# Kernel tuning notes

Measured on AMD Instinct MI355X. Metric: run time of the kernel, lower is better.

## Reference

```python
import jax, jax.numpy as jnp
import numpy as np

EPS = 1e-5

def layer_norm(x, gamma, beta):
    mu = jnp.mean(x, axis=-1, keepdims=True)
    var = jnp.var(x, axis=-1, keepdims=True)
    return (x - mu) * jax.lax.rsqrt(var + EPS) * gamma + beta

def setup_inputs() -> dict:
    key = jax.random.key(0)
    ks = jax.random.split(key, 9)
    B, S, H = 4, 4096, 1024
    x = jax.random.normal(ks[0], (B, S, H), dtype=jnp.float32)
    w1 = jax.random.normal(ks[1], (H, 4 * H), dtype=jnp.float32) * (1.0 / np.sqrt(H))
    b1 = jnp.zeros((4 * H,), dtype=jnp.float32)
    w2 = jax.random.normal(ks[2], (4 * H, H), dtype=jnp.float32) * (1.0 / np.sqrt(4 * H))
    b2 = jnp.zeros((H,), dtype=jnp.float32)
    g1 = jnp.ones((H,), dtype=jnp.float32)
    be1 = jnp.zeros((H,), dtype=jnp.float32)
    g2 = jnp.ones((H,), dtype=jnp.float32)
    be2 = jnp.zeros((H,), dtype=jnp.float32)
    return {"x": x, "w1": w1, "b1": b1, "w2": w2, "b2": b2,
            "g1": g1, "be1": be1, "g2": g2, "be2": be2}

def reference(x, w1, b1, w2, b2, g1, be1, g2, be2):
    # FNet mixing: FFT over hidden dim, then seq dim, take real part
    x_ft = jnp.fft.fft(jnp.fft.fft(x.astype(jnp.float32), axis=-1), axis=-2).real
    h = layer_norm(x + x_ft, g1, be1)
    # FFN with exact GELU (torch nn.GELU default); dropout is identity in eval
    ffn = jax.nn.gelu(h @ w1 + b1, approximate=False) @ w2 + b2
    return layer_norm(h + ffn, g2, be2)
```

## Files before the change

### kernel.cpp

```cpp
#include <hip/hip_runtime.h>
#include <math.h>
#include <stdint.h>

#define DI __device__ __forceinline__
typedef unsigned short u16;
typedef unsigned int   u32;
typedef unsigned long long u64;

typedef __attribute__((ext_vector_type(4))) float f32x4;
typedef __attribute__((ext_vector_type(8))) short bf16x8;

DI float bf2f(u16 v){ return __uint_as_float(((u32)v) << 16); }
DI u16 f2bf(float f){ u32 u = __float_as_uint(f); return (u16)((u + 0x7FFFu + ((u >> 16) & 1u)) >> 16); }
DI u32 pack2(float re, float im){ return (u32)f2bf(re) | ((u32)f2bf(im) << 16); }

DI float gelu_fast(float v){
  float t = v * v;
  float z = v * fmaf(0.0356774081f, t, 0.7978845608f);
  z = fminf(z, 15.0f);
  float e = __expf(2.0f * z);
  return v * e * __frcp_rn(1.0f + e);
}

__global__ __launch_bounds__(256) void transpose_u32(const u32* __restrict__ in, u32* __restrict__ out, int R, int C){
  __shared__ u32 tile[64][65];
  int t = threadIdx.x;
  int c = t & 63, r0 = t >> 6;
  size_t bofs = (size_t)blockIdx.z * (size_t)R * (size_t)C;
  const u32* ib = in  + bofs + (size_t)(blockIdx.y * 64) * C + blockIdx.x * 64;
  u32*       ob = out + bofs + (size_t)(blockIdx.x * 64) * R + blockIdx.y * 64;
  #pragma unroll
  for (int i = 0; i < 16; i++){ int r = r0 + i * 4; tile[r][c] = ib[(size_t)r * C + c]; }
  __syncthreads();
  #pragma unroll
  for (int i = 0; i < 16; i++){ int r = r0 + i * 4; ob[(size_t)r * R + c] = tile[c][r]; }
}

__global__ __launch_bounds__(256) void transpose_f32_bf16(const float* __restrict__ in, u16* __restrict__ out, int R, int C){
  __shared__ u16 tile[64][65];
  int t = threadIdx.x;
  int c = t & 63, r0 = t >> 6;
  const float* ib = in  + (size_t)(blockIdx.y * 64) * C + blockIdx.x * 64;
  u16*         ob = out + (size_t)(blockIdx.x * 64) * R + blockIdx.y * 64;
  #pragma unroll
  for (int i = 0; i < 16; i++){ int r = r0 + i * 4; tile[r][c] = f2bf(ib[(size_t)r * C + c]); }
  __syncthreads();
  #pragma unroll
  for (int i = 0; i < 16; i++){ int r = r0 + i * 4; ob[(size_t)r * R + c] = tile[c][r]; }
}

template<int LOGN>
DI float2* fft_r4(float2* s, float2* d, int t){
  const int Q = 1 << (LOGN - 2);
  #pragma unroll
  for (int st = 0; st < (LOGN >> 1); ++st){
    const int m = 1 << (2 * st);
    const float ang = -6.28318530717958647692f * (float)m / (float)(1 << LOGN);
    #pragma unroll
    for (int j0 = 0; j0 < Q; j0 += 256){
      int j = j0 + t;
      int p = j >> (2 * st);
      int q = j & (m - 1);
      int o = q + (p << (2 * st + 2));
      float2 a0 = s[j], a1 = s[j + Q], a2 = s[j + 2 * Q], a3 = s[j + 3 * Q];
      float s0r = a0.x + a2.x, s0i = a0.y + a2.y, d0r = a0.x - a2.x, d0i = a0.y - a2.y;
      float s1r = a1.x + a3.x, s1i = a1.y + a3.y, d1r = a1.x - a3.x, d1i = a1.y - a3.y;
      float sn, cs; __sincosf(ang * (float)p, &sn, &cs);
      float t2r = cs * cs - sn * sn, t2i = 2.f * cs * sn;
      float t3r = t2r * cs - t2i * sn, t3i = t2r * sn + t2i * cs;
      float e1r = d0r + d1i, e1i = d0i - d1r;
      float e2r = s0r - s1r, e2i = s0i - s1i;
      float e3r = d0r - d1i, e3i = d0i + d1r;
      d[o]         = make_float2(s0r + s1r, s0i + s1i);
      d[o + m]     = make_float2(cs * e1r - sn * e1i,  cs * e1i + sn * e1r);
      d[o + 2 * m] = make_float2(t2r * e2r - t2i * e2i, t2r * e2i + t2i * e2r);
      d[o + 3 * m] = make_float2(t3r * e3r - t3i * e3i, t3r * e3i + t3i * e3r);
    }
    __syncthreads();
    float2* tp = s; s = d; d = tp;
  }
  return s;
}

__global__ __launch_bounds__(256) void fft_seq(const float* __restrict__ xT, u32* __restrict__ ZT2,
                                               float* __restrict__ Zny){
  __shared__ float2 A[4096], Bb[4096];
  int t = threadIdx.x, g = blockIdx.x;
  const float* r0 = xT + (size_t)(2 * g) * 4096;
  #pragma unroll
  for (int i = 0; i < 4; i++){
    int idx = i * 1024 + t * 4;
    float4 va = *(const float4*)(r0 + idx);
    float4 vb = *(const float4*)(r0 + 4096 + idx);
    A[idx + 0] = make_float2(va.x, vb.x);
    A[idx + 1] = make_float2(va.y, vb.y);
    A[idx + 2] = make_float2(va.z, vb.z);
    A[idx + 3] = make_float2(va.w, vb.w);
  }
  __syncthreads();
  float2* R = fft_r4<12>(A, Bb, t);
  size_t ob0 = (size_t)(2 * g) * 2048;
  #pragma unroll
  for (int i = 0; i < 2; i++){
    int k0 = i * 1024 + t * 4;
    u32 wa[4], wb[4];
    #pragma unroll
    for (int kk = 0; kk < 4; kk++){
      int k = k0 + kk, m = (4096 - k) & 4095;
      float2 zk = R[k], zm = R[m];
      wa[kk] = pack2(0.5f * (zk.x + zm.x), 0.5f * (zk.y - zm.y));
      wb[kk] = pack2(0.5f * (zk.y + zm.y), 0.5f * (zm.x - zk.x));
    }
    *(uint4*)(ZT2 + ob0 + k0)        = make_uint4(wa[0], wa[1], wa[2], wa[3]);
    *(uint4*)(ZT2 + ob0 + 2048 + k0) = make_uint4(wb[0], wb[1], wb[2], wb[3]);
  }
  if (t == 0){ float2 z = R[2048]; Zny[2 * g] = z.x; Zny[2 * g + 1] = z.y; }
}

DI void block_stats4(float a1, float a2, float b1, float b2, int t,
                     float& mA, float& iA, float& mB, float& iB){
  __shared__ float sh[4][4];
  #pragma unroll
  for (int o = 32; o > 0; o >>= 1){
    a1 += __shfl_down(a1, o); a2 += __shfl_down(a2, o);
    b1 += __shfl_down(b1, o); b2 += __shfl_down(b2, o);
  }
  if ((t & 63) == 0){ int w = t >> 6; sh[w][0] = a1; sh[w][1] = a2; sh[w][2] = b1; sh[w][3] = b2; }
  __syncthreads();
  float SA = sh[0][0] + sh[1][0] + sh[2][0] + sh[3][0];
  float QA = sh[0][1] + sh[1][1] + sh[2][1] + sh[3][1];
  float SB = sh[0][2] + sh[1][2] + sh[2][2] + sh[3][2];
  float QB = sh[0][3] + sh[1][3] + sh[2][3] + sh[3][3];
  mA = SA * (1.f / 1024.f); iA = rsqrtf(QA * (1.f / 1024.f) - mA * mA + 1e-5f);
  mB = SB * (1.f / 1024.f); iB = rsqrtf(QB * (1.f / 1024.f) - mB * mB + 1e-5f);
}

__global__ __launch_bounds__(256) void fft_hid_ln(const u32* __restrict__ Z2, const float* __restrict__ Zny,
    const float* __restrict__ x, const float* __restrict__ g1, const float* __restrict__ be1,
    u16* __restrict__ h){
  __shared__ float2 A[1024], Bb[1024];
  int t = threadIdx.x, id = blockIdx.x;
  int b = id / 2049, k = id - b * 2049;
  int idx = t * 4;
  if (k == 2048){
    float4 v = *(const float4*)(Zny + b * 1024 + idx);
    A[idx + 0] = make_float2(v.x, 0.f); A[idx + 1] = make_float2(v.y, 0.f);
    A[idx + 2] = make_float2(v.z, 0.f); A[idx + 3] = make_float2(v.w, 0.f);
  } else {
    uint4 zv = *(const uint4*)(Z2 + ((size_t)b * 2048 + k) * 1024 + idx);
    A[idx + 0] = make_float2(bf2f((u16)(zv.x & 0xffffu)), bf2f((u16)(zv.x >> 16)));
    A[idx + 1] = make_float2(bf2f((u16)(zv.y & 0xffffu)), bf2f((u16)(zv.y >> 16)));
    A[idx + 2] = make_float2(bf2f((u16)(zv.z & 0xffffu)), bf2f((u16)(zv.z >> 16)));
    A[idx + 3] = make_float2(bf2f((u16)(zv.w & 0xffffu)), bf2f((u16)(zv.w >> 16)));
  }
  __syncthreads();
  float2* R = fft_r4<10>(A, Bb, t);
  int rowA = b * 4096 + k;
  bool two = (k >= 1) && (k <= 2047);
  int rowB = b * 4096 + (4096 - k);
  float4 xa = *(const float4*)(x + (size_t)rowA * 1024 + idx);
  float vA0 = R[idx + 0].x + xa.x, vA1 = R[idx + 1].x + xa.y;
  float vA2 = R[idx + 2].x + xa.z, vA3 = R[idx + 3].x + xa.w;
  float vB0 = 0.f, vB1 = 0.f, vB2 = 0.f, vB3 = 0.f;
  if (two){
    float4 xb = *(const float4*)(x + (size_t)rowB * 1024 + idx);
    vB0 = R[(1024 - (idx + 0)) & 1023].x + xb.x;
    vB1 = R[(1024 - (idx + 1)) & 1023].x + xb.y;
    vB2 = R[(1024 - (idx + 2)) & 1023].x + xb.z;
    vB3 = R[(1024 - (idx + 3)) & 1023].x + xb.w;
  }
  float mA, iA, mB, iB;
  block_stats4(vA0 + vA1 + vA2 + vA3, vA0 * vA0 + vA1 * vA1 + vA2 * vA2 + vA3 * vA3,
               vB0 + vB1 + vB2 + vB3, vB0 * vB0 + vB1 * vB1 + vB2 * vB2 + vB3 * vB3,
               t, mA, iA, mB, iB);
  float4 gv = *(const float4*)(g1 + idx);
  float4 bv = *(const float4*)(be1 + idx);
  ushort4 oA;
  oA.x = f2bf((vA0 - mA) * iA * gv.x + bv.x);
  oA.y = f2bf((vA1 - mA) * iA * gv.y + bv.y);
  oA.z = f2bf((vA2 - mA) * iA * gv.z + bv.z);
  oA.w = f2bf((vA3 - mA) * iA * gv.w + bv.w);
  *(ushort4*)(h + (size_t)rowA * 1024 + idx) = oA;
  if (two){
    ushort4 oB;
    oB.x = f2bf((vB0 - mB) * iB * gv.x + bv.x);
    oB.y = f2bf((vB1 - mB) * iB * gv.y + bv.y);
    oB.z = f2bf((vB2 - mB) * iB * gv.z + bv.z);
    oB.w = f2bf((vB3 - mB) * iB * gv.w + bv.w);
    *(ushort4*)(h + (size_t)rowB * 1024 + idx) = oB;
  }
}

__global__ __launch_bounds__(256) void ln_rows(const u16* __restrict__ yv, const float* __restrict__ g,
    const float* __restrict__ be, float* __restrict__ o){
  int t = threadIdx.x;
  size_t base = (size_t)blockIdx.x * 1024;
  int idx = t * 4;
  ushort4 v4 = *(const ushort4*)(yv + base + idx);
  float v0 = bf2f(v4.x), v1 = bf2f(v4.y), v2 = bf2f(v4.z), v3 = bf2f(v4.w);
  float mA, iA, mB, iB;
  block_stats4(v0 + v1 + v2 + v3, v0 * v0 + v1 * v1 + v2 * v2 + v3 * v3, 0.f, 0.f, t, mA, iA, mB, iB);
  float4 gv = *(const float4*)(g + idx);
  float4 bv = *(const float4*)(be + idx);
  float4 ov;
  ov.x = (v0 - mA) * iA * gv.x + bv.x;
  ov.y = (v1 - mA) * iA * gv.y + bv.y;
  ov.z = (v2 - mA) * iA * gv.z + bv.z;
  ov.w = (v3 - mA) * iA * gv.w + bv.w;
  *(float4*)(o + base + idx) = ov;
}

typedef const __attribute__((address_space(1))) void* as1cp;
typedef __attribute__((address_space(3))) void* as3p;
DI void async_copy16(const void* g, void* l){
  __builtin_amdgcn_global_load_lds((as1cp)(u64)g, (as3p)(u32)(u64)l, 16, 0, 0);
}
DI void bar(){
  asm volatile("" ::: "memory");
  __builtin_amdgcn_s_barrier();
  asm volatile("" ::: "memory");
}

template<int DOGELU>
__global__ __launch_bounds__(512, 2) void gemm256(const u16* __restrict__ A, const u16* __restrict__ Bm,
    const float* __restrict__ bias, const u16* __restrict__ resid, u16* __restrict__ C,
    int M, int N, int K, int npg_shift)
{
  __shared__ u16 sA[2][2][8192];
  __shared__ u16 sB[2][2][8192];
  int t = threadIdx.x, wv = t >> 6, ln = t & 63;

  int bid = blockIdx.x;
  int c8 = bid & 7, j = bid >> 3;
  int ng = c8 & 3, mh = c8 >> 2;
  int npg = 1 << npg_shift;
  int mph = (M >> 8) >> 1;
  int n0 = (((ng << npg_shift) + (j & (npg - 1))) << 8);
  int m0 = ((mh * mph + (j >> npg_shift)) << 8);

  int wm = wv >> 2, wn = wv & 3;
  int lt = ln & 15;
  int cs = (((ln >> 4) ^ ((ln >> 1) & 3)) << 3);
  int arow = (wm * 128 + lt) * 32 + cs;
  int brow = (wn * 64 + lt) * 32 + cs;

  int srow = wv * 32 + (ln >> 2);
  int gch  = ((ln & 3) ^ ((srow >> 1) & 3)) << 3;
  const u16* gA0 = A  + (size_t)(m0 + srow) * K + gch;
  const u16* gA1 = gA0 + (size_t)16 * K;
  const u16* gB0 = Bm + (size_t)(n0 + srow) * K + gch;
  const u16* gB1 = gB0 + (size_t)16 * K;
  int ldof = wv * 1024 + ln * 8;

  #define STAGE(g0, g1, kc, unit) do{ \
    async_copy16((g0) + (kc), (unit) + ldof); \
    async_copy16((g1) + (kc), (unit) + 512 + ldof); }while(0)

  f32x4 acc[8][4];
  #pragma unroll
  for (int mf = 0; mf < 8; mf++)
    #pragma unroll
    for (int nf = 0; nf < 4; nf++) acc[mf][nf] = (f32x4){0.f, 0.f, 0.f, 0.f};

  int NT = K >> 6;

  STAGE(gA0, gA1, 0,  &sA[0][0][0]);
  STAGE(gB0, gB1, 0,  &sB[0][0][0]);
  STAGE(gA0, gA1, 32, &sA[0][1][0]);
  STAGE(gB0, gB1, 32, &sB[0][1][0]);
  STAGE(gA0, gA1, 64, &sA[1][0][0]);
  STAGE(gB0, gB1, 64, &sB[1][0][0]);
  STAGE(gA0, gA1, 96, &sA[1][1][0]);
  asm volatile("s_waitcnt vmcnt(6)" ::: "memory");
  bar();

  for (int kt = 0; kt < NT; ++kt){
    int buf = kt & 1;
    u16* a0s = &sA[buf][0][0];
    u16* a1s = &sA[buf][1][0];
    u16* b0s = &sB[buf][0][0];
    u16* b1s = &sB[buf][1][0];
    u16* bn1 = &sB[buf ^ 1][1][0];
    bool st1 = (kt + 1) < NT;
    bool st2 = (kt + 2) < NT;
    int kb1 = (kt + 1) << 6, kb2 = (kt + 2) << 6;
    bf16x8 af[8], b0r, b1r, b2r, b3r;

    #pragma unroll
    for (int mf = 0; mf < 8; mf++) af[mf] = *(const bf16x8*)(a0s + arow + mf * 512);
    b0r = *(const bf16x8*)(b0s + brow);
    b1r = *(const bf16x8*)(b0s + brow + 512);
    if (st1) STAGE(gB0, gB1, kb1 + 32, bn1);
    bar();
    __builtin_amdgcn_s_setprio(1);
    #pragma unroll
    for (int mf = 0; mf < 8; mf++){
      acc[mf][0] = __builtin_amdgcn_mfma_f32_16x16x32_bf16(af[mf], b0r, acc[mf][0], 0, 0, 0);
      acc[mf][1] = __builtin_amdgcn_mfma_f32_16x16x32_bf16(af[mf], b1r, acc[mf][1], 0, 0, 0);
    }
    __builtin_amdgcn_s_setprio(0);
    bar();

    b2r = *(const bf16x8*)(b0s + brow + 1024);
    b3r = *(const bf16x8*)(b0s + brow + 1536);
    if (st2) STAGE(gA0, gA1, kb2, a0s);
    bar();
    __builtin_amdgcn_s_setprio(1);
    #pragma unroll
    for (int mf = 0; mf < 8; mf++){
      acc[mf][2] = __builtin_amdgcn_mfma_f32_16x16x32_bf16(af[mf], b2r, acc[mf][2], 0, 0, 0);
      acc[mf][3] = __builtin_amdgcn_mfma_f32_16x16x32_bf16(af[mf], b3r, acc[mf][3], 0, 0, 0);
    }
    __builtin_amdgcn_s_setprio(0);
    bar();

    #pragma unroll
    for (int mf = 0; mf < 8; mf++) af[mf] = *(const bf16x8*)(a1s + arow + mf * 512);
    b0r = *(const bf16x8*)(b1s + brow);
    b1r = *(const bf16x8*)(b1s + brow + 512);
    if (st2) STAGE(gB0, gB1, kb2, b0s);
    bar();
    __builtin_amdgcn_s_setprio(1);
    #pragma unroll
    for (int mf = 0; mf < 8; mf++){
      acc[mf][0] = __builtin_amdgcn_mfma_f32_16x16x32_bf16(af[mf], b0r, acc[mf][0], 0, 0, 0);
      acc[mf][1] = __builtin_amdgcn_mfma_f32_16x16x32_bf16(af[mf], b1r, acc[mf][1], 0, 0, 0);
    }
    __builtin_amdgcn_s_setprio(0);
    bar();

    b2r = *(const bf16x8*)(b1s + brow + 1024);
    b3r = *(const bf16x8*)(b1s + brow + 1536);
    if (st2) STAGE(gA0, gA1, kb2 + 32, a1s);
    bar();
    __builtin_amdgcn_s_setprio(1);
    #pragma unroll
    for (int mf = 0; mf < 8; mf++){
      acc[mf][2] = __builtin_amdgcn_mfma_f32_16x16x32_bf16(af[mf], b2r, acc[mf][2], 0, 0, 0);
      acc[mf][3] = __builtin_amdgcn_mfma_f32_16x16x32_bf16(af[mf], b3r, acc[mf][3], 0, 0, 0);
    }
    __builtin_amdgcn_s_setprio(0);
    if (st2) asm volatile("s_waitcnt vmcnt(6)" ::: "memory");
    else     asm volatile("s_waitcnt vmcnt(0)" ::: "memory");
    bar();
  }
  #undef STAGE

  int colq = lt, rq = ln >> 4;
  #pragma unroll
  for (int mf = 0; mf < 8; mf++){
    int mr = m0 + wm * 128 + mf * 16 + rq * 4;
    #pragma unroll
    for (int nf = 0; nf < 4; nf++){
      int col = n0 + wn * 64 + nf * 16 + colq;
      float bv = bias[col];
      #pragma unroll
      for (int i = 0; i < 4; i++){
        float v = acc[mf][nf][i] + bv;
        if (DOGELU){
          v = gelu_fast(v);
        } else {
          v += bf2f(resid[(size_t)(mr + i) * N + col]);
        }
        C[(size_t)(mr + i) * N + col] = f2bf(v);
      }
    }
  }
}

extern "C" void kernel_launch(void* const* d_in, const int* in_sizes, int n_in,
                              void* d_out, int out_size, void* d_ws, size_t ws_size,
                              hipStream_t stream){
  const float* x   = (const float*)d_in[0];
  const float* w1  = (const float*)d_in[1];
  const float* b1  = (const float*)d_in[2];
  const float* w2  = (const float*)d_in[3];
  const float* b2  = (const float*)d_in[4];
  const float* g1  = (const float*)d_in[5];
  const float* be1 = (const float*)d_in[6];
  const float* g2  = (const float*)d_in[7];
  const float* be2 = (const float*)d_in[8];
  float* out = (float*)d_out;
  char* ws = (char*)d_ws;
  const size_t MB = (size_t)1 << 20;
  float* xT  = (float*)(ws);
  u32*  ZT2  = (u32*)(ws + 64 * MB);
  float* Zny = (float*)(ws + 96 * MB);
  u32*  Z2   = (u32*)(ws);
  u16*  h    = (u16*)(ws + 32 * MB);
  u16*  w1T  = (u16*)(ws + 64 * MB);
  u16*  w2T  = (u16*)(ws + 72 * MB);
  u16*  u    = (u16*)(ws + 80 * MB);
  u16*  y    = (u16*)(ws);
  dim3 blk(256, 1, 1);
  dim3 blk2(512, 1, 1);

  transpose_u32<<<dim3(16, 64, 4), blk, 0, stream>>>((const u32*)x, (u32*)xT, 4096, 1024);
  fft_seq      <<<dim3(2048, 1, 1), blk, 0, stream>>>(xT, ZT2, Zny);
  transpose_u32<<<dim3(32, 16, 4), blk, 0, stream>>>(ZT2, Z2, 1024, 2048);
  fft_hid_ln   <<<dim3(4 * 2049, 1, 1), blk, 0, stream>>>(Z2, Zny, x, g1, be1, h);

  transpose_f32_bf16<<<dim3(64, 16, 1), blk, 0, stream>>>(w1, w1T, 1024, 4096);
  transpose_f32_bf16<<<dim3(16, 64, 1), blk, 0, stream>>>(w2, w2T, 4096, 1024);
  int nch = (ws_size >= (size_t)209 * MB) ? 1 : (ws_size >= (size_t)145 * MB) ? 2 : 4;
  int Mc = 16384 / nch;
  for (int ch = 0; ch < nch; ++ch){
    const u16* hch = h + (size_t)ch * Mc * 1024;
    u16* ych = y + (size_t)ch * Mc * 1024;
    gemm256<1><<<dim3((Mc / 256) * 16), blk2, 0, stream>>>(hch, w1T, b1, (const u16*)nullptr, u, Mc, 4096, 1024, 2);
    gemm256<0><<<dim3((Mc / 256) * 4),  blk2, 0, stream>>>(u, w2T, b2, hch, ych, Mc, 1024, 4096, 0);
  }
  ln_rows<<<dim3(16384, 1, 1), blk, 0, stream>>>(y, g2, be2, out);
}
```

Measured before the change: 548.5 us.

## Make GEMM kernels persistent with a 256-block grid looping over tiles

Turns the two FFN GEMM launches into persistent-style kernels: the grid is capped at 256 blocks and each block loops over several 256x256 output tiles, with a reworked grouping of tile indices by XCD (gn_shift, mpg, bpg). The goal is to cut the tail wave and block launch cost and to keep neighbouring tiles on the same XCD for L2 reuse. The trade-off is that the prologue and epilogue within each block run serially per tile with no overlap between tiles. It also relies on the tile count dividing evenly by the grid.

New measurement: 552.2 us. About the same (+0.7%).

```diff
diff --git a/kernel.cpp b/kernel.cpp
--- a/kernel.cpp
+++ b/kernel.cpp
@@ -224,149 +224,153 @@
 template<int DOGELU>
 __global__ __launch_bounds__(512, 2) void gemm256(const u16* __restrict__ A, const u16* __restrict__ Bm,
     const float* __restrict__ bias, const u16* __restrict__ resid, u16* __restrict__ C,
-    int M, int N, int K, int npg_shift)
+    int M, int N, int K, int gn_shift, int npg_shift, int mpg, int bpg, int npt)
 {
   __shared__ u16 sA[2][2][8192];
   __shared__ u16 sB[2][2][8192];
   int t = threadIdx.x, wv = t >> 6, ln = t & 63;
 
   int bid = blockIdx.x;
-  int c8 = bid & 7, j = bid >> 3;
-  int ng = c8 & 3, mh = c8 >> 2;
-  int npg = 1 << npg_shift;
-  int mph = (M >> 8) >> 1;
-  int n0 = (((ng << npg_shift) + (j & (npg - 1))) << 8);
-  int m0 = ((mh * mph + (j >> npg_shift)) << 8);
+  int c8 = bid & 7, j0 = bid >> 3;
+  int ng = c8 & ((1 << gn_shift) - 1);
+  int mg = c8 >> gn_shift;
+  int npg_m1 = (1 << npg_shift) - 1;
 
   int wm = wv >> 2, wn = wv & 3;
   int lt = ln & 15;
   int cs = (((ln >> 4) ^ ((ln >> 1) & 3)) << 3);
   int arow = (wm * 128 + lt) * 32 + cs;
   int brow = (wn * 64 + lt) * 32 + cs;
-
   int srow = wv * 32 + (ln >> 2);
   int gch  = ((ln & 3) ^ ((srow >> 1) & 3)) << 3;
-  const u16* gA0 = A  + (size_t)(m0 + srow) * K + gch;
-  const u16* gA1 = gA0 + (size_t)16 * K;
-  const u16* gB0 = Bm + (size_t)(n0 + srow) * K + gch;
-  const u16* gB1 = gB0 + (size_t)16 * K;
   int ldof = wv * 1024 + ln * 8;
+  int NT = K >> 6;
 
   #define STAGE(g0, g1, kc, unit) do{ \
     async_copy16((g0) + (kc), (unit) + ldof); \
     async_copy16((g1) + (kc), (unit) + 512 + ldof); }while(0)
 
-  f32x4 acc[8][4];
-  #pragma unroll
-  for (int mf = 0; mf < 8; mf++)
+  for (int s = 0; s < npt; ++s){
+    int jt = j0 + s * bpg;
+    int n0 = (((ng << npg_shift) + (jt & npg_m1)) << 8);
+    int m0 = ((mg * mpg + (jt >> npg_shift)) << 8);
+    const u16* gA0 = A  + (size_t)(m0 + srow) * K + gch;
+    const u16* gA1 = gA0 + (size_t)16 * K;
+    const u16* gB0 = Bm + (size_t)(n0 + srow) * K + gch;
+    const u16* gB1 = gB0 + (size_t)16 * K;
+
+    f32x4 acc[8][4];
     #pragma unroll
-    for (int nf = 0; nf < 4; nf++) acc[mf][nf] = (f32x4){0.f, 0.f, 0.f, 0.f};
-
-  int NT = K >> 6;
-
-  STAGE(gA0, gA1, 0,  &sA[0][0][0]);
-  STAGE(gB0, gB1, 0,  &sB[0][0][0]);
-  STAGE(gA0, gA1, 32, &sA[0][1][0]);
-  STAGE(gB0, gB1, 32, &sB[0][1][0]);
-  STAGE(gA0, gA1, 64, &sA[1][0][0]);
-  STAGE(gB0, gB1, 64, &sB[1][0][0]);
-  STAGE(gA0, gA1, 96, &sA[1][1][0]);
-  asm volatile("s_waitcnt vmcnt(6)" ::: "memory");
-  bar();
-
-  for (int kt = 0; kt < NT; ++kt){
-    int buf = kt & 1;
-    u16* a0s = &sA[buf][0][0];
-    u16* a1s = &sA[buf][1][0];
-    u16* b0s = &sB[buf][0][0];
-    u16* b1s = &sB[buf][1][0];
-    u16* bn1 = &sB[buf ^ 1][1][0];
-    bool st1 = (kt + 1) < NT;
-    bool st2 = (kt + 2) < NT;
-    int kb1 = (kt + 1) << 6, kb2 = (kt + 2) << 6;
-    bf16x8 af[8], b0r, b1r, b2r, b3r;
-
-    #pragma unroll
-    for (int mf = 0; mf < 8; mf++) af[mf] = *(const bf16x8*)(a0s + arow + mf * 512);
-    b0r = *(const bf16x8*)(b0s + brow);
-    b1r = *(const bf16x8*)(b0s + brow + 512);
-    if (st1) STAGE(gB0, gB1, kb1 + 32, bn1);
+    for (int mf = 0; mf < 8; mf++)
+      #pragma unroll
+      for (int nf = 0; nf < 4; nf++) acc[mf][nf] = (f32x4){0.f, 0.f, 0.f, 0.f};
+
+    STAGE(gA0, gA1, 0,  &sA[0][0][0]);
+    STAGE(gB0, gB1, 0,  &sB[0][0][0]);
+    STAGE(gA0, gA1, 32, &sA[0][1][0]);
+    STAGE(gB0, gB1, 32, &sB[0][1][0]);
+    STAGE(gA0, gA1, 64, &sA[1][0][0]);
+    STAGE(gB0, gB1, 64, &sB[1][0][0]);
+    STAGE(gA0, gA1, 96, &sA[1][1][0]);
+    asm volatile("s_waitcnt vmcnt(6)" ::: "memory");
     bar();
-    __builtin_amdgcn_s_setprio(1);
+
+    for (int kt = 0; kt < NT; ++kt){
+      int buf = kt & 1;
+      u16* a0s = &sA[buf][0][0];
+      u16* a1s = &sA[buf][1][0];
+      u16* b0s = &sB[buf][0][0];
+      u16* b1s = &sB[buf][1][0];
+      u16* bn1 = &sB[buf ^ 1][1][0];
+      bool st1 = (kt + 1) < NT;
+      bool st2 = (kt + 2) < NT;
+      int kb1 = (kt + 1) << 6, kb2 = (kt + 2) << 6;
+      bf16x8 af[8], b0r, b1r, b2r, b3r;
+
+      #pragma unroll
+      for (int mf = 0; mf < 8; mf++) af[mf] = *(const bf16x8*)(a0s + arow + mf * 512);
+      b0r = *(const bf16x8*)(b0s + brow);
+      b1r = *(const bf16x8*)(b0s + brow + 512);
+      if (st1) STAGE(gB0, gB1, kb1 + 32, bn1);
+      bar();
+      __builtin_amdgcn_s_setprio(1);
+      #pragma unroll
+      for (int mf = 0; mf < 8; mf++){
+        acc[mf][0] = __builtin_amdgcn_mfma_f32_16x16x32_bf16(af[mf], b0r, acc[mf][0], 0, 0, 0);
+        acc[mf][1] = __builtin_amdgcn_mfma_f32_16x16x32_bf16(af[mf], b1r, acc[mf][1], 0, 0, 0);
+      }
+      __builtin_amdgcn_s_setprio(0);
+      bar();
+
+      b2r = *(const bf16x8*)(b0s + brow + 1024);
+      b3r = *(const bf16x8*)(b0s + brow + 1536);
+      if (st2) STAGE(gA0, gA1, kb2, a0s);
+      bar();
+      __builtin_amdgcn_s_setprio(1);
+      #pragma unroll
+      for (int mf = 0; mf < 8; mf++){
+        acc[mf][2] = __builtin_amdgcn_mfma_f32_16x16x32_bf16(af[mf], b2r, acc[mf][2], 0, 0, 0);
+        acc[mf][3] = __builtin_amdgcn_mfma_f32_16x16x32_bf16(af[mf], b3r, acc[mf][3], 0, 0, 0);
+      }
+      __builtin_amdgcn_s_setprio(0);
+      bar();
+
+      #pragma unroll
+      for (int mf = 0; mf < 8; mf++) af[mf] = *(const bf16x8*)(a1s + arow + mf * 512);
+      b0r = *(const bf16x8*)(b1s + brow);
+      b1r = *(const bf16x8*)(b1s + brow + 512);
+      if (st2) STAGE(gB0, gB1, kb2, b0s);
+      bar();
+      __builtin_amdgcn_s_setprio(1);
+      #pragma unroll
+      for (int mf = 0; mf < 8; mf++){
+        acc[mf][0] = __builtin_amdgcn_mfma_f32_16x16x32_bf16(af[mf], b0r, acc[mf][0], 0, 0, 0);
+        acc[mf][1] = __builtin_amdgcn_mfma_f32_16x16x32_bf16(af[mf], b1r, acc[mf][1], 0, 0, 0);
+      }
+      __builtin_amdgcn_s_setprio(0);
+      bar();
+
+      b2r = *(const bf16x8*)(b1s + brow + 1024);
+      b3r = *(const bf16x8*)(b1s + brow + 1536);
+      if (st2) STAGE(gA0, gA1, kb2 + 32, a1s);
+      bar();
+      __builtin_amdgcn_s_setprio(1);
+      #pragma unroll
+      for (int mf = 0; mf < 8; mf++){
+        acc[mf][2] = __builtin_amdgcn_mfma_f32_16x16x32_bf16(af[mf], b2r, acc[mf][2], 0, 0, 0);
+        acc[mf][3] = __builtin_amdgcn_mfma_f32_16x16x32_bf16(af[mf], b3r, acc[mf][3], 0, 0, 0);
+      }
+      __builtin_amdgcn_s_setprio(0);
+      if (st2) asm volatile("s_waitcnt vmcnt(6)" ::: "memory");
+      else     asm volatile("s_waitcnt vmcnt(0)" ::: "memory");
+      bar();
+    }
+
+    int colq = lt, rq = ln >> 4;
     #pragma unroll
     for (int mf = 0; mf < 8; mf++){
-      acc[mf][0] = __builtin_amdgcn_mfma_f32_16x16x32_bf16(af[mf], b0r, acc[mf][0], 0, 0, 0);
-      acc[mf][1] = __builtin_amdgcn_mfma_f32_16x16x32_bf16(af[mf], b1r, acc[mf][1], 0, 0, 0);
-    }
-    __builtin_amdgcn_s_setprio(0);
-    bar();
-
-    b2r = *(const bf16x8*)(b0s + brow + 1024);
-    b3r = *(const bf16x8*)(b0s + brow + 1536);
-    if (st2) STAGE(gA0, gA1, kb2, a0s);
-    bar();
-    __builtin_amdgcn_s_setprio(1);
-    #pragma unroll
-    for (int mf = 0; mf < 8; mf++){
-      acc[mf][2] = __builtin_amdgcn_mfma_f32_16x16x32_bf16(af[mf], b2r, acc[mf][2], 0, 0, 0);
-      acc[mf][3] = __builtin_amdgcn_mfma_f32_16x16x32_bf16(af[mf], b3r, acc[mf][3], 0, 0, 0);
-    }
-    __builtin_amdgcn_s_setprio(0);
-    bar();
-
-    #pragma unroll
-    for (int mf = 0; mf < 8; mf++) af[mf] = *(const bf16x8*)(a1s + arow + mf * 512);
-    b0r = *(const bf16x8*)(b1s + brow);
-    b1r = *(const bf16x8*)(b1s + brow + 512);
-    if (st2) STAGE(gB0, gB1, kb2, b0s);
-    bar();
-    __builtin_amdgcn_s_setprio(1);
-    #pragma unroll
-    for (int mf = 0; mf < 8; mf++){
-      acc[mf][0] = __builtin_amdgcn_mfma_f32_16x16x32_bf16(af[mf], b0r, acc[mf][0], 0, 0, 0);
-      acc[mf][1] = __builtin_amdgcn_mfma_f32_16x16x32_bf16(af[mf], b1r, acc[mf][1], 0, 0, 0);
-    }
-    __builtin_amdgcn_s_setprio(0);
-    bar();
-
-    b2r = *(const bf16x8*)(b1s + brow + 1024);
-    b3r = *(const bf16x8*)(b1s + brow + 1536);
-    if (st2) STAGE(gA0, gA1, kb2 + 32, a1s);
-    bar();
-    __builtin_amdgcn_s_setprio(1);
-    #pragma unroll
-    for (int mf = 0; mf < 8; mf++){
-      acc[mf][2] = __builtin_amdgcn_mfma_f32_16x16x32_bf16(af[mf], b2r, acc[mf][2], 0, 0, 0);
-      acc[mf][3] = __builtin_amdgcn_mfma_f32_16x16x32_bf16(af[mf], b3r, acc[mf][3], 0, 0, 0);
-    }
-    __builtin_amdgcn_s_setprio(0);
-    if (st2) asm volatile("s_waitcnt vmcnt(6)" ::: "memory");
-    else     asm volatile("s_waitcnt vmcnt(0)" ::: "memory");
-    bar();
+      int mr = m0 + wm * 128 + mf * 16 + rq * 4;
+      #pragma unroll
+      for (int nf = 0; nf < 4; nf++){
+        int col = n0 + wn * 64 + nf * 16 + colq;
+        float bv = bias[col];
+        #pragma unroll
+        for (int i = 0; i < 4; i++){
+          float v = acc[mf][nf][i] + bv;
+          if (DOGELU){
+            v = gelu_fast(v);
+          } else {
+            v += bf2f(resid[(size_t)(mr + i) * N + col]);
+          }
+          C[(size_t)(mr + i) * N + col] = f2bf(v);
+        }
+      }
+    }
   }
   #undef STAGE
-
-  int colq = lt, rq = ln >> 4;
-  #pragma unroll
-  for (int mf = 0; mf < 8; mf++){
-    int mr = m0 + wm * 128 + mf * 16 + rq * 4;
-    #pragma unroll
-    for (int nf = 0; nf < 4; nf++){
-      int col = n0 + wn * 64 + nf * 16 + colq;
-      float bv = bias[col];
-      #pragma unroll
-      for (int i = 0; i < 4; i++){
-        float v = acc[mf][nf][i] + bv;
-        if (DOGELU){
-          v = gelu_fast(v);
-        } else {
-          v += bf2f(resid[(size_t)(mr + i) * N + col]);
-        }
-        C[(size_t)(mr + i) * N + col] = f2bf(v);
-      }
-    }
-  }
-}
+}
+
+static inline int ilog2(int v){ int s = 0; while ((1 << s) < v) ++s; return s; }
 
 extern "C" void kernel_launch(void* const* d_in, const int* in_sizes, int n_in,
                               void* d_out, int out_size, void* d_ws, size_t ws_size,
@@ -407,8 +411,26 @@
   for (int ch = 0; ch < nch; ++ch){
     const u16* hch = h + (size_t)ch * Mc * 1024;
     u16* ych = y + (size_t)ch * Mc * 1024;
-    gemm256<1><<<dim3((Mc / 256) * 16), blk2, 0, stream>>>(hch, w1T, b1, (const u16*)nullptr, u, Mc, 4096, 1024, 2);
-    gemm256<0><<<dim3((Mc / 256) * 4),  blk2, 0, stream>>>(u, w2T, b2, hch, ych, Mc, 1024, 4096, 0);
+    {
+      int tm = Mc >> 8, tn = 16, gn = 2;
+      int tiles = tm * tn;
+      int grid = tiles < 256 ? tiles : 256;
+      int npt = tiles / grid, bpg = grid >> 3;
+      int npgs = ilog2(tn >> gn);
+      int mpg = tm >> (3 - gn);
+      gemm256<1><<<dim3(grid), blk2, 0, stream>>>(hch, w1T, b1, (const u16*)nullptr, u,
+                                                  Mc, 4096, 1024, gn, npgs, mpg, bpg, npt);
+    }
+    {
+      int tm = Mc >> 8, tn = 4, gn = 0;
+      int tiles = tm * tn;
+      int grid = tiles < 256 ? tiles : 256;
+      int npt = tiles / grid, bpg = grid >> 3;
+      int npgs = ilog2(tn >> gn);
+      int mpg = tm >> (3 - gn);
+      gemm256<0><<<dim3(grid), blk2, 0, stream>>>(u, w2T, b2, hch, ych,
+                                                  Mc, 1024, 4096, gn, npgs, mpg, bpg, npt);
+    }
   }
   ln_rows<<<dim3(16384, 1, 1), blk, 0, stream>>>(y, g2, be2, out);
 }
```
